# Kernel tuning notes

Hardware: AMD Instinct MI355X
Metric: run time of the kernel (lower is better)

The kernel has to match this reference:

```python
import jax, jax.numpy as jnp
import numpy as np

TEMPERATURE = 8.0  # sqrt(d_k) with d_k = 64


def setup_inputs() -> dict:
    key = jax.random.key(0)
    kq, kk, kv, km = jax.random.split(key, 4)
    B, S, D = 32, 2048, 64
    q = jax.random.normal(kq, (B, S, D), dtype=jnp.float32)
    k = jax.random.normal(kk, (B, S, D), dtype=jnp.float32)
    v = jax.random.normal(kv, (B, S, D), dtype=jnp.float32)
    mask = jax.random.randint(km, (B, S, S), 0, 2).astype(jnp.bool_)
    return {"q": q, "k": k, "v": v, "mask": mask}


def reference(q, k, v, mask):
    # scores: [B, S, S] = q @ k^T, mask -> -inf, scale by 1/temperature
    scores = jnp.einsum("bqd,bkd->bqk", q, k)
    scores = jnp.where(mask, -jnp.inf, scores) / TEMPERATURE
    attn = jax.nn.softmax(scores, axis=2)
    output = jnp.einsum("bqk,bkd->bqd", attn, v)
    return (output, attn)
```

## Files before the change

### kernel.cpp

```cpp
#include <hip/hip_runtime.h>
#include <hip/hip_bf16.h>

typedef __attribute__((ext_vector_type(8))) short short8;
typedef __attribute__((ext_vector_type(4))) short short4b;
typedef __attribute__((ext_vector_type(4))) float f32x4;

#define S_LEN 2048
#define DIM   64
#define BR    64
#define BC    64
#define NKT   (S_LEN / BC)

#define KP  72
#define BP  33
#define AP  68

__device__ __forceinline__ short f2bf(float f) {
    __hip_bfloat16 h = __float2bfloat16(f);
    return __builtin_bit_cast(short, h);
}

__global__ __launch_bounds__(256, 3)
void sdpa_kernel(const float* __restrict__ q, const float* __restrict__ k,
                 const float* __restrict__ v, const int* __restrict__ mask,
                 float* __restrict__ out, float* __restrict__ attn)
{
    __shared__ __align__(16) short Klds[BR * KP];
    __shared__ __align__(16) short Vtlds[DIM * KP];
    __shared__ __align__(16) unsigned long long Bits[BR * BP];
    __shared__ __align__(16) float Albs[BR * AP];

    const int t  = threadIdx.x;
    const int l  = t & 63;
    const int wv = t >> 6;
    const int lg = l >> 4;
    const int ll = l & 15;

    const int wg = blockIdx.x;
    const int b  = wg >> 5;
    const int i0 = (wg & 31) * BR;

    const float LOG2E_T = 0.18033688011112042f;

    short8 qf[2];
    {
        const float* qrow = q + ((size_t)(b * S_LEN + i0 + 16 * wv + ll) * DIM);
        #pragma unroll
        for (int s = 0; s < 2; ++s) {
            const float* p = qrow + s * 32 + lg * 8;
            float4 a = *(const float4*)p;
            float4 c = *(const float4*)(p + 4);
            short8 f;
            f[0]=f2bf(a.x); f[1]=f2bf(a.y); f[2]=f2bf(a.z); f[3]=f2bf(a.w);
            f[4]=f2bf(c.x); f[5]=f2bf(c.y); f[6]=f2bf(c.z); f[7]=f2bf(c.w);
            qf[s] = f;
        }
    }

    float rs[4] = {0.f, 0.f, 0.f, 0.f};

    for (int kt = 0; kt < NKT; ++kt) {
        const int j0 = kt * BC;

        #pragma unroll
        for (int p = 0; p < 4; ++p) {
            int row = (t >> 4) + p * 16;
            int dd  = (t & 15) * 4;
            float4 kv4 = *(const float4*)(k + ((size_t)(b * S_LEN + j0 + row) * DIM + dd));
            short4b s4;
            s4[0]=f2bf(kv4.x); s4[1]=f2bf(kv4.y); s4[2]=f2bf(kv4.z); s4[3]=f2bf(kv4.w);
            *(short4b*)&Klds[row * KP + dd] = s4;
        }

        {
            const int* mrow = mask + (size_t)(b * S_LEN + i0 + 16 * wv) * S_LEN + j0 + l;
            int mv[16];
            #pragma unroll
            for (int r = 0; r < 16; ++r)
                mv[r] = __builtin_nontemporal_load(mrow + (size_t)r * S_LEN);
            unsigned long long myword = 0ull;
            #pragma unroll
            for (int r = 0; r < 16; ++r) {
                unsigned long long bal = __ballot(mv[r] != 0);
                if (ll == r) myword = bal;
            }
            if (l < 16) Bits[(16 * wv + l) * BP + kt] = myword;
        }
        __syncthreads();

        unsigned long long wbits[4];
        #pragma unroll
        for (int r = 0; r < 4; ++r)
            wbits[r] = Bits[(16 * wv + lg * 4 + r) * BP + kt];

        #pragma unroll
        for (int jt = 0; jt < 4; ++jt) {
            short8 b0 = *(short8*)&Klds[(jt * 16 + ll) * KP + lg * 8];
            short8 b1 = *(short8*)&Klds[(jt * 16 + ll) * KP + 32 + lg * 8];
            f32x4 c = {0.f, 0.f, 0.f, 0.f};
            c = __builtin_amdgcn_mfma_f32_16x16x32_bf16(qf[0], b0, c, 0, 0, 0);
            c = __builtin_amdgcn_mfma_f32_16x16x32_bf16(qf[1], b1, c, 0, 0, 0);
            #pragma unroll
            for (int r = 0; r < 4; ++r) {
                unsigned int bit = (unsigned int)(wbits[r] >> (jt * 16 + ll)) & 1u;
                float pexp = bit ? 0.f : __builtin_amdgcn_exp2f(c[r] * LOG2E_T);
                rs[r] += pexp;
            }
        }
        __syncthreads();
    }

    float inv[4];
    #pragma unroll
    for (int r = 0; r < 4; ++r) {
        float s = rs[r];
        s += __shfl_xor(s, 1);
        s += __shfl_xor(s, 2);
        s += __shfl_xor(s, 4);
        s += __shfl_xor(s, 8);
        inv[r] = 1.0f / s;
    }

    f32x4 oacc[4];
    #pragma unroll
    for (int dt = 0; dt < 4; ++dt) oacc[dt] = (f32x4){0.f, 0.f, 0.f, 0.f};

    for (int kt = 0; kt < NKT; ++kt) {
        const int j0 = kt * BC;

        #pragma unroll
        for (int p = 0; p < 4; ++p) {
            int row = (t >> 4) + p * 16;
            int dd  = (t & 15) * 4;
            float4 kv4 = *(const float4*)(k + ((size_t)(b * S_LEN + j0 + row) * DIM + dd));
            short4b s4;
            s4[0]=f2bf(kv4.x); s4[1]=f2bf(kv4.y); s4[2]=f2bf(kv4.z); s4[3]=f2bf(kv4.w);
            *(short4b*)&Klds[row * KP + dd] = s4;
        }
        #pragma unroll
        for (int it = 0; it < 8; ++it) {
            int jp = (t >> 4) + (it & 1) * 16;
            int dd = (t & 15) + (it >> 1) * 16;
            const float* vp = v + ((size_t)(b * S_LEN + j0 + jp * 2) * DIM + dd);
            float v0 = vp[0];
            float v1 = vp[DIM];
            unsigned int pk = (unsigned int)(unsigned short)f2bf(v0) |
                              ((unsigned int)(unsigned short)f2bf(v1) << 16);
            *(unsigned int*)&Vtlds[dd * KP + jp * 2] = pk;
        }
        __syncthreads();

        unsigned long long wbits[4];
        #pragma unroll
        for (int r = 0; r < 4; ++r)
            wbits[r] = Bits[(16 * wv + lg * 4 + r) * BP + kt];

        #pragma unroll
        for (int jt = 0; jt < 4; ++jt) {
            short8 b0 = *(short8*)&Klds[(jt * 16 + ll) * KP + lg * 8];
            short8 b1 = *(short8*)&Klds[(jt * 16 + ll) * KP + 32 + lg * 8];
            f32x4 c = {0.f, 0.f, 0.f, 0.f};
            c = __builtin_amdgcn_mfma_f32_16x16x32_bf16(qf[0], b0, c, 0, 0, 0);
            c = __builtin_amdgcn_mfma_f32_16x16x32_bf16(qf[1], b1, c, 0, 0, 0);
            #pragma unroll
            for (int r = 0; r < 4; ++r) {
                unsigned int bit = (unsigned int)(wbits[r] >> (jt * 16 + ll)) & 1u;
                float pexp = bit ? 0.f : __builtin_amdgcn_exp2f(c[r] * LOG2E_T);
                float pn = pexp * inv[r];
                Albs[(16 * wv + lg * 4 + r) * AP + jt * 16 + ll] = pn;
            }
        }

        short8 paf[2];
        #pragma unroll
        for (int s = 0; s < 2; ++s) {
            const float* ap = &Albs[(16 * wv + ll) * AP + s * 32 + lg * 8];
            float4 x = *(const float4*)ap;
            float4 y = *(const float4*)(ap + 4);
            short8 f;
            f[0]=f2bf(x.x); f[1]=f2bf(x.y); f[2]=f2bf(x.z); f[3]=f2bf(x.w);
            f[4]=f2bf(y.x); f[5]=f2bf(y.y); f[6]=f2bf(y.z); f[7]=f2bf(y.w);
            paf[s] = f;
        }

        #pragma unroll
        for (int dt = 0; dt < 4; ++dt) {
            short8 b0 = *(short8*)&Vtlds[(dt * 16 + ll) * KP + lg * 8];
            short8 b1 = *(short8*)&Vtlds[(dt * 16 + ll) * KP + 32 + lg * 8];
            oacc[dt] = __builtin_amdgcn_mfma_f32_16x16x32_bf16(paf[0], b0, oacc[dt], 0, 0, 0);
            oacc[dt] = __builtin_amdgcn_mfma_f32_16x16x32_bf16(paf[1], b1, oacc[dt], 0, 0, 0);
        }

        {
            float* abase = attn + (size_t)b * S_LEN * S_LEN;
            #pragma unroll
            for (int ps = 0; ps < 4; ++ps) {
                int row = 16 * wv + lg + ps * 4;
                f32x4 val = *(f32x4*)&Albs[row * AP + ll * 4];
                float* dst = abase + (size_t)(i0 + row) * S_LEN + j0 + ll * 4;
                __builtin_nontemporal_store(val, (f32x4*)dst);
            }
        }
        __syncthreads();
    }

    #pragma unroll
    for (int dt = 0; dt < 4; ++dt)
        #pragma unroll
        for (int r = 0; r < 4; ++r)
            out[(size_t)(b * S_LEN + i0 + 16 * wv + lg * 4 + r) * DIM + dt * 16 + ll] = oacc[dt][r];
}

extern "C" void kernel_launch(void* const* d_in, const int* in_sizes, int n_in,
                              void* d_out, int out_size, void* d_ws, size_t ws_size,
                              hipStream_t stream) {
    const float* q    = (const float*)d_in[0];
    const float* k    = (const float*)d_in[1];
    const float* v    = (const float*)d_in[2];
    const int*   mask = (const int*)d_in[3];
    float* out  = (float*)d_out;
    float* attn = out + (size_t)32 * S_LEN * DIM;
    sdpa_kernel<<<dim3(32 * (S_LEN / BR)), dim3(256), 0, stream>>>(q, k, v, mask, out, attn);
}
```

Baseline: 318.2 us.

## Pre-convert K and transposed V to bf16 in workspace, read directly from global

Adds two prepass kernels that convert K to bf16 and V to a transposed bf16 layout in the workspace. The main kernel then loads MFMA operands straight from global or L2 instead of staging through LDS with barriers. It also keeps mask bits in registers via ballot/shuffle rather than an LDS bit table, raises the occupancy hint to 4, and remaps blocks so each XCD handles whole batches for L2 locality. The original kernel stays as a fallback when workspace is too small, at the cost of two extra launches and extra global traffic.

```diff
diff --git a/kernel.cpp b/kernel.cpp
--- a/kernel.cpp
+++ b/kernel.cpp
@@ -7,6 +7,7 @@
 
 #define S_LEN 2048
 #define DIM   64
+#define NB    32
 #define BR    64
 #define BC    64
 #define NKT   (S_LEN / BC)
@@ -20,14 +21,53 @@
     return __builtin_bit_cast(short, h);
 }
 
-__global__ __launch_bounds__(256, 3)
-void sdpa_kernel(const float* __restrict__ q, const float* __restrict__ k,
-                 const float* __restrict__ v, const int* __restrict__ mask,
-                 float* __restrict__ out, float* __restrict__ attn)
+
+__global__ __launch_bounds__(256)
+void conv_k_kernel(const float* __restrict__ k, short* __restrict__ kbf)
 {
-    __shared__ __align__(16) short Klds[BR * KP];
-    __shared__ __align__(16) short Vtlds[DIM * KP];
-    __shared__ __align__(16) unsigned long long Bits[BR * BP];
+    size_t idx = ((size_t)blockIdx.x * 256 + threadIdx.x) * 8;
+    const float* p = k + idx;
+    float4 a = *(const float4*)p;
+    float4 c = *(const float4*)(p + 4);
+    short8 f;
+    f[0]=f2bf(a.x); f[1]=f2bf(a.y); f[2]=f2bf(a.z); f[3]=f2bf(a.w);
+    f[4]=f2bf(c.x); f[5]=f2bf(c.y); f[6]=f2bf(c.z); f[7]=f2bf(c.w);
+    *(short8*)(kbf + idx) = f;
+}
+
+__global__ __launch_bounds__(256)
+void conv_vt_kernel(const float* __restrict__ v, short* __restrict__ vtb)
+{
+    __shared__ float tile[64][65];
+    const int t  = threadIdx.x;
+    const int b  = blockIdx.x >> 5;
+    const int j0 = (blockIdx.x & 31) * 64;
+
+    #pragma unroll
+    for (int p = 0; p < 4; ++p) {
+        int j = (t >> 4) + p * 16;
+        int d = (t & 15) * 4;
+        float4 x = *(const float4*)(v + ((size_t)(b * S_LEN + j0 + j) * DIM + d));
+        tile[j][d+0]=x.x; tile[j][d+1]=x.y; tile[j][d+2]=x.z; tile[j][d+3]=x.w;
+    }
+    __syncthreads();
+    #pragma unroll
+    for (int p = 0; p < 4; ++p) {
+        int d  = (t >> 4) + p * 16;
+        int j4 = (t & 15) * 4;
+        short4b s4;
+        s4[0]=f2bf(tile[j4+0][d]); s4[1]=f2bf(tile[j4+1][d]);
+        s4[2]=f2bf(tile[j4+2][d]); s4[3]=f2bf(tile[j4+3][d]);
+        *(short4b*)(vtb + ((size_t)(b * DIM + d) * S_LEN + j0 + j4)) = s4;
+    }
+}
+
+
+__global__ __launch_bounds__(256, 4)
+void sdpa_fast(const float* __restrict__ q, const int* __restrict__ mask,
+               const short* __restrict__ kbf, const short* __restrict__ vtb,
+               float* __restrict__ out, float* __restrict__ attn)
+{
     __shared__ __align__(16) float Albs[BR * AP];
 
     const int t  = threadIdx.x;
@@ -36,9 +76,11 @@
     const int lg = l >> 4;
     const int ll = l & 15;
 
-    const int wg = blockIdx.x;
-    const int b  = wg >> 5;
-    const int i0 = (wg & 31) * BR;
+    const int bx  = blockIdx.x;
+    const int xcd = bx & 7;
+    const int kk  = bx >> 3;
+    const int b   = xcd * 4 + (kk >> 5);
+    const int i0  = (kk & 31) * BR;
 
     const float LOG2E_T = 0.18033688011112042f;
 
@@ -58,10 +100,169 @@
     }
 
     float rs[4] = {0.f, 0.f, 0.f, 0.f};
+    unsigned long long w8[8];
+
+    for (int o = 0; o < 4; ++o) {
+        #pragma unroll
+        for (int u = 0; u < 8; ++u) {
+            const int kt = 8 * o + u;
+            const int j0 = kt * BC;
+
+            const int* mrow = mask + (size_t)(b * S_LEN + i0 + 16 * wv) * S_LEN + j0 + l;
+            int mv[16];
+            #pragma unroll
+            for (int r = 0; r < 16; ++r)
+                mv[r] = __builtin_nontemporal_load(mrow + (size_t)r * S_LEN);
+
+            unsigned long long wb[4];
+            #pragma unroll
+            for (int r = 0; r < 16; ++r) {
+                unsigned long long bal = __ballot(mv[r] != 0);
+                if ((r >> 2) == lg) wb[r & 3] = bal;
+                if (lg == o && ll == r) w8[u] = bal;
+            }
+
+            #pragma unroll
+            for (int jt = 0; jt < 4; ++jt) {
+                const short* kbase = kbf + ((size_t)(b * S_LEN + j0 + jt * 16 + ll) * DIM);
+                short8 b0 = *(const short8*)(kbase + lg * 8);
+                short8 b1 = *(const short8*)(kbase + 32 + lg * 8);
+                f32x4 c = {0.f, 0.f, 0.f, 0.f};
+                c = __builtin_amdgcn_mfma_f32_16x16x32_bf16(qf[0], b0, c, 0, 0, 0);
+                c = __builtin_amdgcn_mfma_f32_16x16x32_bf16(qf[1], b1, c, 0, 0, 0);
+                #pragma unroll
+                for (int r = 0; r < 4; ++r) {
+                    unsigned int bit = (unsigned int)(wb[r] >> (jt * 16 + ll)) & 1u;
+                    rs[r] += bit ? 0.f : __builtin_amdgcn_exp2f(c[r] * LOG2E_T);
+                }
+            }
+        }
+    }
+
+    float inv[4];
+    #pragma unroll
+    for (int r = 0; r < 4; ++r) {
+        float s = rs[r];
+        s += __shfl_xor(s, 1);
+        s += __shfl_xor(s, 2);
+        s += __shfl_xor(s, 4);
+        s += __shfl_xor(s, 8);
+        inv[r] = 1.0f / s;
+    }
+
+    f32x4 oacc[4];
+    #pragma unroll
+    for (int dt = 0; dt < 4; ++dt) oacc[dt] = (f32x4){0.f, 0.f, 0.f, 0.f};
+
+    float* const abase = attn + (size_t)b * S_LEN * S_LEN;
+
+    for (int o = 0; o < 4; ++o) {
+        #pragma unroll
+        for (int u = 0; u < 8; ++u) {
+            const int kt = 8 * o + u;
+            const int j0 = kt * BC;
+
+            unsigned long long wb[4];
+            #pragma unroll
+            for (int r = 0; r < 4; ++r)
+                wb[r] = __shfl(w8[u], 16 * o + lg * 4 + r);
+
+            #pragma unroll
+            for (int jt = 0; jt < 4; ++jt) {
+                const short* kbase = kbf + ((size_t)(b * S_LEN + j0 + jt * 16 + ll) * DIM);
+                short8 b0 = *(const short8*)(kbase + lg * 8);
+                short8 b1 = *(const short8*)(kbase + 32 + lg * 8);
+                f32x4 c = {0.f, 0.f, 0.f, 0.f};
+                c = __builtin_amdgcn_mfma_f32_16x16x32_bf16(qf[0], b0, c, 0, 0, 0);
+                c = __builtin_amdgcn_mfma_f32_16x16x32_bf16(qf[1], b1, c, 0, 0, 0);
+                #pragma unroll
+                for (int r = 0; r < 4; ++r) {
+                    unsigned int bit = (unsigned int)(wb[r] >> (jt * 16 + ll)) & 1u;
+                    float pexp = bit ? 0.f : __builtin_amdgcn_exp2f(c[r] * LOG2E_T);
+                    Albs[(16 * wv + lg * 4 + r) * AP + jt * 16 + ll] = pexp * inv[r];
+                }
+            }
+
+            short8 paf[2];
+            #pragma unroll
+            for (int s = 0; s < 2; ++s) {
+                const float* ap = &Albs[(16 * wv + ll) * AP + s * 32 + lg * 8];
+                float4 x = *(const float4*)ap;
+                float4 y = *(const float4*)(ap + 4);
+                short8 f;
+                f[0]=f2bf(x.x); f[1]=f2bf(x.y); f[2]=f2bf(x.z); f[3]=f2bf(x.w);
+                f[4]=f2bf(y.x); f[5]=f2bf(y.y); f[6]=f2bf(y.z); f[7]=f2bf(y.w);
+                paf[s] = f;
+            }
+
+            #pragma unroll
+            for (int dt = 0; dt < 4; ++dt) {
+                const short* vbase = vtb + ((size_t)(b * DIM + dt * 16 + ll) * S_LEN) + j0;
+                short8 b0 = *(const short8*)(vbase + lg * 8);
+                short8 b1 = *(const short8*)(vbase + 32 + lg * 8);
+                oacc[dt] = __builtin_amdgcn_mfma_f32_16x16x32_bf16(paf[0], b0, oacc[dt], 0, 0, 0);
+                oacc[dt] = __builtin_amdgcn_mfma_f32_16x16x32_bf16(paf[1], b1, oacc[dt], 0, 0, 0);
+            }
+
+            #pragma unroll
+            for (int ps = 0; ps < 4; ++ps) {
+                int row = 16 * wv + lg + ps * 4;
+                f32x4 val = *(f32x4*)&Albs[row * AP + ll * 4];
+                float* dst = abase + (size_t)(i0 + row) * S_LEN + j0 + ll * 4;
+                __builtin_nontemporal_store(val, (f32x4*)dst);
+            }
+        }
+    }
+
+    #pragma unroll
+    for (int dt = 0; dt < 4; ++dt)
+        #pragma unroll
+        for (int r = 0; r < 4; ++r)
+            out[(size_t)(b * S_LEN + i0 + 16 * wv + lg * 4 + r) * DIM + dt * 16 + ll] = oacc[dt][r];
+}
+
+
+__global__ __launch_bounds__(256, 3)
+void sdpa_fb(const float* __restrict__ q, const float* __restrict__ k,
+             const float* __restrict__ v, const int* __restrict__ mask,
+             float* __restrict__ out, float* __restrict__ attn)
+{
+    __shared__ __align__(16) short Klds[BR * KP];
+    __shared__ __align__(16) short Vtlds[DIM * KP];
+    __shared__ __align__(16) unsigned long long Bits[BR * BP];
+    __shared__ __align__(16) float Albs[BR * AP];
+
+    const int t  = threadIdx.x;
+    const int l  = t & 63;
+    const int wv = t >> 6;
+    const int lg = l >> 4;
+    const int ll = l & 15;
+
+    const int wg = blockIdx.x;
+    const int b  = wg >> 5;
+    const int i0 = (wg & 31) * BR;
+
+    const float LOG2E_T = 0.18033688011112042f;
+
+    short8 qf[2];
+    {
+        const float* qrow = q + ((size_t)(b * S_LEN + i0 + 16 * wv + ll) * DIM);
+        #pragma unroll
+        for (int s = 0; s < 2; ++s) {
+            const float* p = qrow + s * 32 + lg * 8;
+            float4 a = *(const float4*)p;
+            float4 c = *(const float4*)(p + 4);
+            short8 f;
+            f[0]=f2bf(a.x); f[1]=f2bf(a.y); f[2]=f2bf(a.z); f[3]=f2bf(a.w);
+            f[4]=f2bf(c.x); f[5]=f2bf(c.y); f[6]=f2bf(c.z); f[7]=f2bf(c.w);
+            qf[s] = f;
+        }
+    }
+
+    float rs[4] = {0.f, 0.f, 0.f, 0.f};
 
     for (int kt = 0; kt < NKT; ++kt) {
         const int j0 = kt * BC;
-
         #pragma unroll
         for (int p = 0; p < 4; ++p) {
             int row = (t >> 4) + p * 16;
@@ -71,7 +272,6 @@
             s4[0]=f2bf(kv4.x); s4[1]=f2bf(kv4.y); s4[2]=f2bf(kv4.z); s4[3]=f2bf(kv4.w);
             *(short4b*)&Klds[row * KP + dd] = s4;
         }
-
         {
             const int* mrow = mask + (size_t)(b * S_LEN + i0 + 16 * wv) * S_LEN + j0 + l;
             int mv[16];
@@ -103,8 +303,7 @@
             #pragma unroll
             for (int r = 0; r < 4; ++r) {
                 unsigned int bit = (unsigned int)(wbits[r] >> (jt * 16 + ll)) & 1u;
-                float pexp = bit ? 0.f : __builtin_amdgcn_exp2f(c[r] * LOG2E_T);
-                rs[r] += pexp;
+                rs[r] += bit ? 0.f : __builtin_amdgcn_exp2f(c[r] * LOG2E_T);
             }
         }
         __syncthreads();
@@ -127,7 +326,6 @@
 
     for (int kt = 0; kt < NKT; ++kt) {
         const int j0 = kt * BC;
-
         #pragma unroll
         for (int p = 0; p < 4; ++p) {
             int row = (t >> 4) + p * 16;
@@ -166,8 +364,7 @@
             for (int r = 0; r < 4; ++r) {
                 unsigned int bit = (unsigned int)(wbits[r] >> (jt * 16 + ll)) & 1u;
                 float pexp = bit ? 0.f : __builtin_amdgcn_exp2f(c[r] * LOG2E_T);
-                float pn = pexp * inv[r];
-                Albs[(16 * wv + lg * 4 + r) * AP + jt * 16 + ll] = pn;
+                Albs[(16 * wv + lg * 4 + r) * AP + jt * 16 + ll] = pexp * inv[r];
             }
         }
 
@@ -219,6 +416,18 @@
     const float* v    = (const float*)d_in[2];
     const int*   mask = (const int*)d_in[3];
     float* out  = (float*)d_out;
-    float* attn = out + (size_t)32 * S_LEN * DIM;
-    sdpa_kernel<<<dim3(32 * (S_LEN / BR)), dim3(256), 0, stream>>>(q, k, v, mask, out, attn);
-}
+    float* attn = out + (size_t)NB * S_LEN * DIM;
+
+    const size_t nel = (size_t)NB * S_LEN * DIM;
+    const size_t ws_needed = 2 * nel * sizeof(short);
+
+    if (ws_size >= ws_needed) {
+        short* kbf = (short*)d_ws;
+        short* vtb = kbf + nel;
+        conv_k_kernel<<<dim3(nel / (256 * 8)), dim3(256), 0, stream>>>(k, kbf);
+        conv_vt_kernel<<<dim3(NB * 32), dim3(256), 0, stream>>>(v, vtb);
+        sdpa_fast<<<dim3(NB * (S_LEN / BR)), dim3(256), 0, stream>>>(q, mask, kbf, vtb, out, attn);
+    } else {
+        sdpa_fb<<<dim3(NB * (S_LEN / BR)), dim3(256), 0, stream>>>(q, k, v, mask, out, attn);
+    }
+}
```

Result: slower. 417.6 us (+31.2%).
